# Kernel tuning notes

Measured on AMD Instinct MI355X. Metric: run time of the kernel, lower is better.

## Reference

```python
import jax, jax.numpy as jnp
import numpy as np

B, S, H, I, E, K = 4, 2048, 1024, 4096, 8, 2


def setup_inputs() -> dict:
    key = jax.random.key(0)
    ks = jax.random.split(key, 5)
    scale = 1.0 / np.sqrt(H)
    return {
        "hidden_states": jax.random.normal(ks[0], (B, S, H), dtype=jnp.float32),
        "router_w": jax.random.normal(ks[1], (E, H), dtype=jnp.float32) * scale,
        "gate_w": jax.random.normal(ks[2], (E, I, H), dtype=jnp.float32) * scale,
        "up_w": jax.random.normal(ks[3], (E, I, H), dtype=jnp.float32) * scale,
        "down_w": jax.random.normal(ks[4], (E, H, I), dtype=jnp.float32) * (1.0 / np.sqrt(I)),
        "top_k": K,
    }


def reference(hidden_states, router_w, gate_w, up_w, down_w, top_k):
    # Router: logits -> softmax -> top-k -> renormalized weights (eval mode, no jitter)
    logits = jnp.einsum("bsh,eh->bse", hidden_states, router_w)
    probs = jax.nn.softmax(logits, axis=-1)
    expert_weights, expert_indices = jax.lax.top_k(probs, top_k)  # [B,S,K]
    expert_weights = expert_weights / expert_weights.sum(axis=-1, keepdims=True)

    n_experts = router_w.shape[0]
    # Per-token combine weight for each expert: [B,S,E]
    combine = (jax.nn.one_hot(expert_indices, n_experts, dtype=expert_weights.dtype)
               * expert_weights[..., None]).sum(axis=-2)

    out = jnp.zeros_like(hidden_states)
    for e in range(n_experts):  # fixed small expert count
        g = jax.nn.silu(hidden_states @ gate_w[e].T)  # [B,S,I]
        u = hidden_states @ up_w[e].T                 # [B,S,I]
        y = (g * u) @ down_w[e].T                     # [B,S,H]
        out = out + combine[..., e:e + 1] * y
    return out
```

## Files before the change

### kernel.cpp

```cpp
#include <hip/hip_runtime.h>
#include <hip/hip_bf16.h>
#include <math.h>
#include <stdint.h>

#define TOKENS 8192
#define HD 1024
#define ID 4096
#define NE 8
#define RMAX 18432
#define MAXT 72

typedef __attribute__((ext_vector_type(8))) short short8v;
typedef __attribute__((ext_vector_type(4))) float f32x4;

typedef const __attribute__((address_space(1))) unsigned int* gas_u32p;
typedef __attribute__((address_space(3))) unsigned int* las_u32p;

__device__ __forceinline__ void stage16(const void* g, void* l) {
  __builtin_amdgcn_global_load_lds((gas_u32p)g, (las_u32p)l, 16, 0, 0);
}

#define BARRIER asm volatile("s_barrier" ::: "memory")
#define WAITLGKM asm volatile("s_waitcnt lgkmcnt(0)" ::: "memory")
#define VMC0 asm volatile("s_waitcnt vmcnt(0)" ::: "memory")
#define VMC4 asm volatile("s_waitcnt vmcnt(4)" ::: "memory")
#define VMC6 asm volatile("s_waitcnt vmcnt(6)" ::: "memory")

__global__ __launch_bounds__(256) void convert_kernel(const float* __restrict__ src,
                                                      __hip_bfloat16* __restrict__ dst) {
  size_t i = ((size_t)blockIdx.x * 256 + threadIdx.x) * 8;
  float4 a = ((const float4*)(src + i))[0];
  float4 b = ((const float4*)(src + i))[1];
  union { __hip_bfloat16 h[8]; int4 v; } u;
  u.h[0] = __float2bfloat16(a.x); u.h[1] = __float2bfloat16(a.y);
  u.h[2] = __float2bfloat16(a.z); u.h[3] = __float2bfloat16(a.w);
  u.h[4] = __float2bfloat16(b.x); u.h[5] = __float2bfloat16(b.y);
  u.h[6] = __float2bfloat16(b.z); u.h[7] = __float2bfloat16(b.w);
  *(int4*)(dst + i) = u.v;
}

__global__ __launch_bounds__(256) void router_kernel(
    const float* __restrict__ h, const float* __restrict__ rw,
    __hip_bfloat16* __restrict__ hx, int* __restrict__ tidx,
    float* __restrict__ tw, int* __restrict__ cnt) {
  int wid = threadIdx.x >> 6, lane = threadIdx.x & 63;
  int t = blockIdx.x * 4 + wid;
  const float4* h4 = (const float4*)(h + (size_t)t * HD);
  float x[16];
  {
    float4 xa = h4[lane * 4 + 0], xb = h4[lane * 4 + 1], xc = h4[lane * 4 + 2], xd = h4[lane * 4 + 3];
    x[0] = xa.x; x[1] = xa.y; x[2] = xa.z; x[3] = xa.w;
    x[4] = xb.x; x[5] = xb.y; x[6] = xb.z; x[7] = xb.w;
    x[8] = xc.x; x[9] = xc.y; x[10] = xc.z; x[11] = xc.w;
    x[12] = xd.x; x[13] = xd.y; x[14] = xd.z; x[15] = xd.w;
  }
  union { __hip_bfloat16 hb[16]; int4 v[2]; } u;
#pragma unroll
  for (int j = 0; j < 16; j++) u.hb[j] = __float2bfloat16(x[j]);
  {
    int4* hxp = (int4*)(hx + (size_t)t * HD + lane * 16);
    hxp[0] = u.v[0]; hxp[1] = u.v[1];
  }
  double acc[NE];
#pragma unroll
  for (int e = 0; e < NE; e++) {
    const float4* w4 = (const float4*)(rw + e * HD);
    float4 wa = w4[lane * 4 + 0], wb = w4[lane * 4 + 1], wc = w4[lane * 4 + 2], wd = w4[lane * 4 + 3];
    double s = 0.0;
    s += (double)x[0] * wa.x + (double)x[1] * wa.y + (double)x[2] * wa.z + (double)x[3] * wa.w;
    s += (double)x[4] * wb.x + (double)x[5] * wb.y + (double)x[6] * wb.z + (double)x[7] * wb.w;
    s += (double)x[8] * wc.x + (double)x[9] * wc.y + (double)x[10] * wc.z + (double)x[11] * wc.w;
    s += (double)x[12] * wd.x + (double)x[13] * wd.y + (double)x[14] * wd.z + (double)x[15] * wd.w;
    acc[e] = s;
  }
#pragma unroll
  for (int off = 32; off >= 1; off >>= 1)
#pragma unroll
    for (int e = 0; e < NE; e++) acc[e] += __shfl_xor(acc[e], off, 64);
  if (lane == 0) {
    int i0 = 0; double l0 = acc[0];
#pragma unroll
    for (int e = 1; e < NE; e++) if (acc[e] > l0) { l0 = acc[e]; i0 = e; }
    int i1 = -1; double l1 = -1.0e300;
#pragma unroll
    for (int e = 0; e < NE; e++) if (e != i0 && acc[e] > l1) { l1 = acc[e]; i1 = e; }
    double r = exp(l1 - l0);
    float w0 = (float)(1.0 / (1.0 + r));
    float w1 = (float)(r / (1.0 + r));
    tidx[t * 2 + 0] = i0; tidx[t * 2 + 1] = i1;
    tw[t * 2 + 0] = w0;  tw[t * 2 + 1] = w1;
    atomicAdd(&cnt[i0], 1); atomicAdd(&cnt[i1], 1);
  }
}

__global__ void scan_kernel(const int* __restrict__ cnt, int* __restrict__ ofs, int* __restrict__ cnt2) {
  if (threadIdx.x == 0) {
    int a = 0;
    for (int e = 0; e < NE; e++) { ofs[e] = a; a += (cnt[e] + 255) & ~255; }
    ofs[NE] = a;
  }
  if (threadIdx.x < NE) cnt2[threadIdx.x] = 0;
}

__global__ __launch_bounds__(256) void scatter_kernel(
    const int* __restrict__ tidx, const float* __restrict__ tw,
    const int* __restrict__ ofs, int* __restrict__ cnt2,
    int* __restrict__ rowmap, int* __restrict__ slots) {
  int t = blockIdx.x * 256 + threadIdx.x;
#pragma unroll
  for (int k = 0; k < 2; k++) {
    int e = tidx[t * 2 + k];
    int pos = atomicAdd(&cnt2[e], 1);
    int row = ofs[e] + pos;
    rowmap[row] = t;
    slots[t * 2 + k] = row;
  }
}

__global__ __launch_bounds__(256) void gather_kernel(
    const __hip_bfloat16* __restrict__ hx, const int* __restrict__ rowmap,
    const int* __restrict__ ofs, __hip_bfloat16* __restrict__ A1) {
  int r = blockIdx.x * 4 + (threadIdx.x >> 6);
  int lane = threadIdx.x & 63;
  if (r >= ofs[NE]) return;
  int t = rowmap[r];
  int4* dst = (int4*)(A1 + (size_t)r * HD);
  if (t < 0) {
    int4 z = {0, 0, 0, 0};
    dst[lane * 2 + 0] = z; dst[lane * 2 + 1] = z;
  } else {
    const int4* src = (const int4*)(hx + (size_t)t * HD);
    dst[lane * 2 + 0] = src[lane * 2 + 0];
    dst[lane * 2 + 1] = src[lane * 2 + 1];
  }
}

#define MFMAQ(ACC, MO, NO, AF, BF)                                                         \
  { _Pragma("unroll") for (int m_ = 0; m_ < 4; m_++)                                       \
    _Pragma("unroll") for (int n_ = 0; n_ < 2; n_++)                                       \
    _Pragma("unroll") for (int k_ = 0; k_ < 2; k_++)                                       \
      ACC[(MO) + m_][(NO) + n_] = __builtin_amdgcn_mfma_f32_16x16x32_bf16(                 \
          AF[m_][k_], BF[n_][k_], ACC[(MO) + m_][(NO) + n_], 0, 0, 0); }

__global__ __launch_bounds__(512, 2) void gemm1_kernel(
    const __hip_bfloat16* __restrict__ A1, const __hip_bfloat16* __restrict__ Wg,
    const __hip_bfloat16* __restrict__ Wu, const int* __restrict__ ofs,
    __hip_bfloat16* __restrict__ act) {
  __shared__ __align__(128) char lds[131072];
  const int nwg = gridDim.x;
  int wg0 = blockIdx.x;
  int wg = (wg0 & 7) * (nwg >> 3) + (wg0 >> 3);
  const int tm = wg >> 5, tn = wg & 31;
  const int Rtot = ofs[NE];
  const int row0 = tm * 256;
  if (row0 >= Rtot) return;
  int e = 0;
#pragma unroll
  for (int i = 1; i < NE; i++) e += (row0 >= ofs[i]);
  const int tid = threadIdx.x, wid = tid >> 6, lane = tid & 63;
  const int wm = wid >> 1, wn = wid & 1;
  const int fr = lane & 15, fkE = (lane >> 4) << 3;
  const int wmB = wm * 64, wnB = wn * 64;

  const char* srcA[4]; const char* srcG[2]; const char* srcU[2];
  int ldA[4], ldG[2], ldU[2];
#pragma unroll
  for (int j = 0; j < 4; j++) {
    int d = j * 8192 + tid * 16;
    int row = d >> 7;
    int kb = (d ^ (((d >> 7) & 7) << 4)) & 127;
    srcA[j] = (const char*)(A1 + (size_t)(row0 + row) * HD) + kb;
    ldA[j] = j * 8192 + wid * 1024;
  }
#pragma unroll
  for (int j = 0; j < 2; j++) {
    int d = j * 8192 + tid * 16;
    int row = d >> 7;
    int kb = (d ^ (((d >> 7) & 7) << 4)) & 127;
    srcG[j] = (const char*)(Wg + ((size_t)e * ID + tn * 128 + row) * HD) + kb;
    srcU[j] = (const char*)(Wu + ((size_t)e * ID + tn * 128 + row) * HD) + kb;
    ldG[j] = 32768 + j * 8192 + wid * 1024;
    ldU[j] = 49152 + j * 8192 + wid * 1024;
  }
#define STG_A(j, t, bf) stage16(srcA[j] + (size_t)(t) * 128, (char*)lds + (bf) * 65536 + ldA[j])
#define STG_G(j, t, bf) stage16(srcG[j] + (size_t)(t) * 128, (char*)lds + (bf) * 65536 + ldG[j])
#define STG_U(j, t, bf) stage16(srcU[j] + (size_t)(t) * 128, (char*)lds + (bf) * 65536 + ldU[j])

  auto RD = [&](int bf, int poff, int rowi, int kki) -> short8v {
    int o = ((rowi + fr) << 7) + ((kki << 5) + fkE) * 2;
    o ^= ((o >> 7) & 7) << 4;
    return *(const short8v*)(&lds[bf * 65536 + poff + o]);
  };

  f32x4 accG[4][4], accU[4][4];
#pragma unroll
  for (int m = 0; m < 4; m++)
#pragma unroll
    for (int n = 0; n < 4; n++) { accG[m][n] = (f32x4)(0.0f); accU[m][n] = (f32x4)(0.0f); }

  const int NT = HD / 64;
#pragma unroll
  for (int j = 0; j < 4; j++) STG_A(j, 0, 0);
#pragma unroll
  for (int j = 0; j < 2; j++) STG_G(j, 0, 0);
#pragma unroll
  for (int j = 0; j < 2; j++) STG_U(j, 0, 0);
#pragma unroll
  for (int j = 0; j < 4; j++) STG_A(j, 1, 1);
#pragma unroll
  for (int j = 0; j < 2; j++) STG_G(j, 1, 1);
  VMC6; BARRIER;

#pragma unroll 1
  for (int I = 0; I < NT / 2; ++I) {
    const int t0 = 2 * I;
    const bool more = (t0 + 2 < NT);
    short8v a[4][2], bA[2][2], bB[2][2];
#pragma unroll
    for (int m = 0; m < 4; m++) { a[m][0] = RD(0, 0, wmB + m * 16, 0); a[m][1] = RD(0, 0, wmB + m * 16, 1); }
#pragma unroll
    for (int n = 0; n < 2; n++) { bA[n][0] = RD(0, 32768, wnB + n * 16, 0); bA[n][1] = RD(0, 32768, wnB + n * 16, 1); }
    STG_U(0, t0 + 1, 1); STG_U(1, t0 + 1, 1);
    BARRIER; WAITLGKM;
    __builtin_amdgcn_s_setprio(1); MFMAQ(accG, 0, 0, a, bA); __builtin_amdgcn_s_setprio(0);
    BARRIER;
#pragma unroll
    for (int n = 0; n < 2; n++) { bB[n][0] = RD(0, 32768, wnB + 32 + n * 16, 0); bB[n][1] = RD(0, 32768, wnB + 32 + n * 16, 1); }
    if (more) { STG_A(0, t0 + 2, 0); STG_A(1, t0 + 2, 0); }
    BARRIER; WAITLGKM;
    __builtin_amdgcn_s_setprio(1); MFMAQ(accG, 0, 2, a, bB); __builtin_amdgcn_s_setprio(0);
    BARRIER;
#pragma unroll
    for (int n = 0; n < 2; n++) { bA[n][0] = RD(0, 49152, wnB + n * 16, 0); bA[n][1] = RD(0, 49152, wnB + n * 16, 1); }
    if (more) { STG_A(2, t0 + 2, 0); STG_A(3, t0 + 2, 0); }
    BARRIER; WAITLGKM;
    __builtin_amdgcn_s_setprio(1); MFMAQ(accU, 0, 0, a, bA); __builtin_amdgcn_s_setprio(0);
    BARRIER;
#pragma unroll
    for (int n = 0; n < 2; n++) { bB[n][0] = RD(0, 49152, wnB + 32 + n * 16, 0); bB[n][1] = RD(0, 49152, wnB + 32 + n * 16, 1); }
    if (more) { STG_G(0, t0 + 2, 0); STG_G(1, t0 + 2, 0); }
    BARRIER; WAITLGKM;
    __builtin_amdgcn_s_setprio(1); MFMAQ(accU, 0, 2, a, bB); __builtin_amdgcn_s_setprio(0);
    if (more) { VMC6; } else { VMC0; }
    BARRIER;
#pragma unroll
    for (int m = 0; m < 4; m++) { a[m][0] = RD(1, 0, wmB + m * 16, 0); a[m][1] = RD(1, 0, wmB + m * 16, 1); }
#pragma unroll
    for (int n = 0; n < 2; n++) { bA[n][0] = RD(1, 32768, wnB + n * 16, 0); bA[n][1] = RD(1, 32768, wnB + n * 16, 1); }
    if (more) { STG_U(0, t0 + 2, 0); STG_U(1, t0 + 2, 0); }
    BARRIER; WAITLGKM;
    __builtin_amdgcn_s_setprio(1); MFMAQ(accG, 0, 0, a, bA); __builtin_amdgcn_s_setprio(0);
    BARRIER;
#pragma unroll
    for (int n = 0; n < 2; n++) { bB[n][0] = RD(1, 32768, wnB + 32 + n * 16, 0); bB[n][1] = RD(1, 32768, wnB + 32 + n * 16, 1); }
    if (more) { STG_A(0, t0 + 3, 1); STG_A(1, t0 + 3, 1); }
    BARRIER; WAITLGKM;
    __builtin_amdgcn_s_setprio(1); MFMAQ(accG, 0, 2, a, bB); __builtin_amdgcn_s_setprio(0);
    BARRIER;
#pragma unroll
    for (int n = 0; n < 2; n++) { bA[n][0] = RD(1, 49152, wnB + n * 16, 0); bA[n][1] = RD(1, 49152, wnB + n * 16, 1); }
    if (more) { STG_A(2, t0 + 3, 1); STG_A(3, t0 + 3, 1); }
    BARRIER; WAITLGKM;
    __builtin_amdgcn_s_setprio(1); MFMAQ(accU, 0, 0, a, bA); __builtin_amdgcn_s_setprio(0);
    BARRIER;
#pragma unroll
    for (int n = 0; n < 2; n++) { bB[n][0] = RD(1, 49152, wnB + 32 + n * 16, 0); bB[n][1] = RD(1, 49152, wnB + 32 + n * 16, 1); }
    if (more) { STG_G(0, t0 + 3, 1); STG_G(1, t0 + 3, 1); }
    BARRIER; WAITLGKM;
    __builtin_amdgcn_s_setprio(1); MFMAQ(accU, 0, 2, a, bB); __builtin_amdgcn_s_setprio(0);
    if (more) { VMC6; } else { VMC0; }
    BARRIER;
  }
#undef STG_A
#undef STG_G
#undef STG_U

  const int rb = row0 + wmB + ((lane >> 4) << 2);
  const int cb = tn * 128 + wnB + fr;
#pragma unroll
  for (int m = 0; m < 4; m++)
#pragma unroll
    for (int i = 0; i < 4; i++) {
      int r = rb + m * 16 + i;
      __hip_bfloat16* dst = act + (size_t)r * ID + cb;
#pragma unroll
      for (int n = 0; n < 4; n++) {
        float g = accG[m][n][i], uu = accU[m][n][i];
        float s = g / (1.0f + __expf(-g));
        dst[n * 16] = __float2bfloat16(s * uu);
      }
    }
}

__global__ __launch_bounds__(512, 2) void gemm2_kernel(
    const __hip_bfloat16* __restrict__ act, const __hip_bfloat16* __restrict__ Wd,
    const int* __restrict__ ofs, float* __restrict__ ybuf) {
  __shared__ __align__(128) char lds[131072];
  const int nwg = gridDim.x;
  int wg0 = blockIdx.x;
  int wg = (wg0 & 7) * (nwg >> 3) + (wg0 >> 3);
  const int tm = wg >> 2, tn = wg & 3;
  const int Rtot = ofs[NE];
  const int row0 = tm * 256;
  if (row0 >= Rtot) return;
  int e = 0;
#pragma unroll
  for (int i = 1; i < NE; i++) e += (row0 >= ofs[i]);
  const int tid = threadIdx.x, wid = tid >> 6, lane = tid & 63;
  const int wm = wid >> 2, wn = wid & 3;
  const int fr = lane & 15, fkE = (lane >> 4) << 3;
  const int wmB = wm * 128, wnB = wn * 64;

  const char* srcA[4]; const char* srcB[4];
  int ldA[4], ldB[4];
#pragma unroll
  for (int j = 0; j < 4; j++) {
    int d = j * 8192 + tid * 16;
    int row = d >> 7;
    int kb = (d ^ (((d >> 7) & 7) << 4)) & 127;
    srcA[j] = (const char*)(act + (size_t)(row0 + row) * ID) + kb;
    srcB[j] = (const char*)(Wd + ((size_t)e * HD + tn * 256 + row) * ID) + kb;
    ldA[j] = j * 8192 + wid * 1024;
    ldB[j] = 32768 + j * 8192 + wid * 1024;
  }
#define STG_A2(j, t, bf) stage16(srcA[j] + (size_t)(t) * 128, (char*)lds + (bf) * 65536 + ldA[j])
#define STG_B2(j, t, bf) stage16(srcB[j] + (size_t)(t) * 128, (char*)lds + (bf) * 65536 + ldB[j])

  auto RD = [&](int bf, int poff, int rowi, int kki) -> short8v {
    int o = ((rowi + fr) << 7) + ((kki << 5) + fkE) * 2;
    o ^= ((o >> 7) & 7) << 4;
    return *(const short8v*)(&lds[bf * 65536 + poff + o]);
  };

  f32x4 acc[8][4];
#pragma unroll
  for (int m = 0; m < 8; m++)
#pragma unroll
    for (int n = 0; n < 4; n++) acc[m][n] = (f32x4)(0.0f);

  const int NT = ID / 64;
#pragma unroll
  for (int j = 0; j < 4; j++) STG_B2(j, 0, 0);
#pragma unroll
  for (int j = 0; j < 4; j++) STG_A2(j, 0, 0);
#pragma unroll
  for (int j = 0; j < 4; j++) STG_B2(j, 1, 1);
  VMC4; BARRIER;

#pragma unroll 1
  for (int I = 0; I < NT / 2; ++I) {
    const int t0 = 2 * I;
    const bool more = (t0 + 2 < NT);
    short8v a0[4][2], a1[4][2], b0[2][2], b1[2][2];
#pragma unroll
    for (int m = 0; m < 4; m++) { a0[m][0] = RD(0, 0, wmB + m * 16, 0); a0[m][1] = RD(0, 0, wmB + m * 16, 1); }
#pragma unroll
    for (int n = 0; n < 2; n++) { b0[n][0] = RD(0, 32768, wnB + n * 16, 0); b0[n][1] = RD(0, 32768, wnB + n * 16, 1); }
    STG_A2(0, t0 + 1, 1); STG_A2(1, t0 + 1, 1);
    BARRIER; WAITLGKM;
    __builtin_amdgcn_s_setprio(1); MFMAQ(acc, 0, 0, a0, b0); __builtin_amdgcn_s_setprio(0);
    BARRIER;
#pragma unroll
    for (int n = 0; n < 2; n++) { b1[n][0] = RD(0, 32768, wnB + 32 + n * 16, 0); b1[n][1] = RD(0, 32768, wnB + 32 + n * 16, 1); }
    STG_A2(2, t0 + 1, 1); STG_A2(3, t0 + 1, 1);
    BARRIER; WAITLGKM;
    __builtin_amdgcn_s_setprio(1); MFMAQ(acc, 0, 2, a0, b1); __builtin_amdgcn_s_setprio(0);
    BARRIER;
#pragma unroll
    for (int m = 0; m < 4; m++) { a1[m][0] = RD(0, 0, wmB + 64 + m * 16, 0); a1[m][1] = RD(0, 0, wmB + 64 + m * 16, 1); }
    if (more) { STG_B2(0, t0 + 2, 0); STG_B2(1, t0 + 2, 0); }
    BARRIER; WAITLGKM;
    __builtin_amdgcn_s_setprio(1); MFMAQ(acc, 4, 2, a1, b1); __builtin_amdgcn_s_setprio(0);
    BARRIER;
    if (more) { STG_B2(2, t0 + 2, 0); STG_B2(3, t0 + 2, 0); }
    BARRIER; WAITLGKM;
    __builtin_amdgcn_s_setprio(1); MFMAQ(acc, 4, 0, a1, b0); __builtin_amdgcn_s_setprio(0);
    if (more) { VMC4; } else { VMC0; }
    BARRIER;
#pragma unroll
    for (int m = 0; m < 4; m++) { a0[m][0] = RD(1, 0, wmB + m * 16, 0); a0[m][1] = RD(1, 0, wmB + m * 16, 1); }
#pragma unroll
    for (int n = 0; n < 2; n++) { b0[n][0] = RD(1, 32768, wnB + n * 16, 0); b0[n][1] = RD(1, 32768, wnB + n * 16, 1); }
    if (more) { STG_A2(0, t0 + 2, 0); STG_A2(1, t0 + 2, 0); }
    BARRIER; WAITLGKM;
    __builtin_amdgcn_s_setprio(1); MFMAQ(acc, 0, 0, a0, b0); __builtin_amdgcn_s_setprio(0);
    BARRIER;
#pragma unroll
    for (int n = 0; n < 2; n++) { b1[n][0] = RD(1, 32768, wnB + 32 + n * 16, 0); b1[n][1] = RD(1, 32768, wnB + 32 + n * 16, 1); }
    if (more) { STG_A2(2, t0 + 2, 0); STG_A2(3, t0 + 2, 0); }
    BARRIER; WAITLGKM;
    __builtin_amdgcn_s_setprio(1); MFMAQ(acc, 0, 2, a0, b1); __builtin_amdgcn_s_setprio(0);
    BARRIER;
#pragma unroll
    for (int m = 0; m < 4; m++) { a1[m][0] = RD(1, 0, wmB + 64 + m * 16, 0); a1[m][1] = RD(1, 0, wmB + 64 + m * 16, 1); }
    if (more) { STG_B2(0, t0 + 3, 1); STG_B2(1, t0 + 3, 1); }
    BARRIER; WAITLGKM;
    __builtin_amdgcn_s_setprio(1); MFMAQ(acc, 4, 2, a1, b1); __builtin_amdgcn_s_setprio(0);
    BARRIER;
    if (more) { STG_B2(2, t0 + 3, 1); STG_B2(3, t0 + 3, 1); }
    BARRIER; WAITLGKM;
    __builtin_amdgcn_s_setprio(1); MFMAQ(acc, 4, 0, a1, b0); __builtin_amdgcn_s_setprio(0);
    if (more) { VMC4; } else { VMC0; }
    BARRIER;
  }
#undef STG_A2
#undef STG_B2

  const int rb = row0 + wmB + ((lane >> 4) << 2);
  const int cb = tn * 256 + wnB + fr;
#pragma unroll
  for (int m = 0; m < 8; m++)
#pragma unroll
    for (int i = 0; i < 4; i++) {
      int r = rb + m * 16 + i;
      float* dst = ybuf + (size_t)r * HD + cb;
#pragma unroll
      for (int n = 0; n < 4; n++) dst[n * 16] = acc[m][n][i];
    }
}

__global__ __launch_bounds__(256) void combine_kernel(
    const float* __restrict__ ybuf, const int* __restrict__ slots,
    const float* __restrict__ tw, float* __restrict__ out) {
  int t = blockIdx.x * 4 + (threadIdx.x >> 6);
  int lane = threadIdx.x & 63;
  int r0 = slots[t * 2 + 0], r1 = slots[t * 2 + 1];
  float w0 = tw[t * 2 + 0], w1 = tw[t * 2 + 1];
  const float4* y0 = (const float4*)(ybuf + (size_t)r0 * HD);
  const float4* y1 = (const float4*)(ybuf + (size_t)r1 * HD);
  float4* o = (float4*)(out + (size_t)t * HD);
#pragma unroll
  for (int j = 0; j < 4; j++) {
    int ix = j * 64 + lane;
    float4 a = y0[ix], b = y1[ix];
    float4 c;
    c.x = w0 * a.x + w1 * b.x; c.y = w0 * a.y + w1 * b.y;
    c.z = w0 * a.z + w1 * b.z; c.w = w0 * a.w + w1 * b.w;
    o[ix] = c;
  }
}

extern "C" void kernel_launch(void* const* d_in, const int* in_sizes, int n_in,
                              void* d_out, int out_size, void* d_ws, size_t ws_size,
                              hipStream_t stream) {
  (void)in_sizes; (void)n_in; (void)out_size; (void)ws_size;
  const float* h  = (const float*)d_in[0];
  const float* rw = (const float*)d_in[1];
  const float* gw = (const float*)d_in[2];
  const float* uw = (const float*)d_in[3];
  const float* dw = (const float*)d_in[4];
  float* out = (float*)d_out;

  char* ws = (char*)d_ws;
  size_t off = 0;
  auto alloc = [&](size_t bytes) { char* p = ws + off; off += (bytes + 255) & ~255ULL; return p; };
  __hip_bfloat16* wg  = (__hip_bfloat16*)alloc((size_t)NE * ID * HD * 2);
  __hip_bfloat16* wu  = (__hip_bfloat16*)alloc((size_t)NE * ID * HD * 2);
  __hip_bfloat16* wd  = (__hip_bfloat16*)alloc((size_t)NE * HD * ID * 2);
  __hip_bfloat16* act = (__hip_bfloat16*)alloc((size_t)RMAX * ID * 2);
  size_t hx_off = off;
  __hip_bfloat16* hx  = (__hip_bfloat16*)alloc((size_t)TOKENS * HD * 2);
  __hip_bfloat16* A1  = (__hip_bfloat16*)alloc((size_t)RMAX * HD * 2);
  float* ybuf = (float*)(ws + hx_off);
  {
    size_t yend = hx_off + (size_t)RMAX * HD * 4;
    if (yend > off) off = (yend + 255) & ~255ULL;
  }
  int* rowmap = (int*)alloc(RMAX * 4);
  int* tidx   = (int*)alloc(TOKENS * 2 * 4);
  float* twt  = (float*)alloc(TOKENS * 2 * 4);
  int* slots  = (int*)alloc(TOKENS * 2 * 4);
  int* cnt    = (int*)alloc(256);
  int* cnt2   = (int*)alloc(256);
  int* ofs    = (int*)alloc(256);

  hipMemsetAsync(cnt, 0, NE * 4, stream);
  hipMemsetAsync(rowmap, 0xFF, RMAX * 4, stream);

  convert_kernel<<<16384, 256, 0, stream>>>(gw, wg);
  convert_kernel<<<16384, 256, 0, stream>>>(uw, wu);
  convert_kernel<<<16384, 256, 0, stream>>>(dw, wd);
  router_kernel<<<TOKENS / 4, 256, 0, stream>>>(h, rw, hx, tidx, twt, cnt);
  scan_kernel<<<1, 64, 0, stream>>>(cnt, ofs, cnt2);
  scatter_kernel<<<TOKENS / 256, 256, 0, stream>>>(tidx, twt, ofs, cnt2, rowmap, slots);
  gather_kernel<<<RMAX / 4, 256, 0, stream>>>(hx, rowmap, ofs, A1);
  gemm1_kernel<<<MAXT * 32, 512, 0, stream>>>(A1, wg, wu, ofs, act);
  gemm2_kernel<<<MAXT * 4, 512, 0, stream>>>(act, wd, ofs, ybuf);
  combine_kernel<<<TOKENS / 4, 256, 0, stream>>>(ybuf, slots, twt, out);
}
```

Baseline: 925.4 us.

## Fuse row gather into gemm1 A loads and shrink gemm2 N tile

Removes the gather kernel and the A1 buffer: gemm1 now builds its A-tile source pointers directly from rowmap into hx, with padded rows pointing at a zeroed row. gemm2's output tile drops from 256x256 to 256x128 with 8 waves in a 4x2 layout. That doubles the grid, halves the accumulators and cuts LDS to 96KB, and its staging pipeline is restructured around a vmcnt(3) wait. The aim is to save one kernel launch plus a full copy of the gathered activations, and to improve gemm2 occupancy and load balance. The cost is that gemm2 rereads the activation tiles from global memory twice as often.

```diff
diff --git a/kernel.cpp b/kernel.cpp
--- a/kernel.cpp
+++ b/kernel.cpp
@@ -23,7 +23,7 @@
 #define BARRIER asm volatile("s_barrier" ::: "memory")
 #define WAITLGKM asm volatile("s_waitcnt lgkmcnt(0)" ::: "memory")
 #define VMC0 asm volatile("s_waitcnt vmcnt(0)" ::: "memory")
-#define VMC4 asm volatile("s_waitcnt vmcnt(4)" ::: "memory")
+#define VMC3 asm volatile("s_waitcnt vmcnt(3)" ::: "memory")
 #define VMC6 asm volatile("s_waitcnt vmcnt(6)" ::: "memory")
 
 __global__ __launch_bounds__(256) void convert_kernel(const float* __restrict__ src,
@@ -117,24 +117,6 @@
   }
 }
 
-__global__ __launch_bounds__(256) void gather_kernel(
-    const __hip_bfloat16* __restrict__ hx, const int* __restrict__ rowmap,
-    const int* __restrict__ ofs, __hip_bfloat16* __restrict__ A1) {
-  int r = blockIdx.x * 4 + (threadIdx.x >> 6);
-  int lane = threadIdx.x & 63;
-  if (r >= ofs[NE]) return;
-  int t = rowmap[r];
-  int4* dst = (int4*)(A1 + (size_t)r * HD);
-  if (t < 0) {
-    int4 z = {0, 0, 0, 0};
-    dst[lane * 2 + 0] = z; dst[lane * 2 + 1] = z;
-  } else {
-    const int4* src = (const int4*)(hx + (size_t)t * HD);
-    dst[lane * 2 + 0] = src[lane * 2 + 0];
-    dst[lane * 2 + 1] = src[lane * 2 + 1];
-  }
-}
-
 #define MFMAQ(ACC, MO, NO, AF, BF)                                                         \
   { _Pragma("unroll") for (int m_ = 0; m_ < 4; m_++)                                       \
     _Pragma("unroll") for (int n_ = 0; n_ < 2; n_++)                                       \
@@ -143,8 +125,9 @@
           AF[m_][k_], BF[n_][k_], ACC[(MO) + m_][(NO) + n_], 0, 0, 0); }
 
 __global__ __launch_bounds__(512, 2) void gemm1_kernel(
-    const __hip_bfloat16* __restrict__ A1, const __hip_bfloat16* __restrict__ Wg,
-    const __hip_bfloat16* __restrict__ Wu, const int* __restrict__ ofs,
+    const __hip_bfloat16* __restrict__ hx, const __hip_bfloat16* __restrict__ Wg,
+    const __hip_bfloat16* __restrict__ Wu, const int* __restrict__ rowmap,
+    const int* __restrict__ ofs, const __hip_bfloat16* __restrict__ zrow,
     __hip_bfloat16* __restrict__ act) {
   __shared__ __align__(128) char lds[131072];
   const int nwg = gridDim.x;
@@ -169,7 +152,9 @@
     int d = j * 8192 + tid * 16;
     int row = d >> 7;
     int kb = (d ^ (((d >> 7) & 7) << 4)) & 127;
-    srcA[j] = (const char*)(A1 + (size_t)(row0 + row) * HD) + kb;
+    int tok = rowmap[row0 + row];
+    const __hip_bfloat16* base = (tok >= 0) ? (hx + (size_t)tok * HD) : zrow;
+    srcA[j] = (const char*)base + kb;
     ldA[j] = j * 8192 + wid * 1024;
   }
 #pragma unroll
@@ -295,11 +280,11 @@
 __global__ __launch_bounds__(512, 2) void gemm2_kernel(
     const __hip_bfloat16* __restrict__ act, const __hip_bfloat16* __restrict__ Wd,
     const int* __restrict__ ofs, float* __restrict__ ybuf) {
-  __shared__ __align__(128) char lds[131072];
+  __shared__ __align__(128) char lds[98304];
   const int nwg = gridDim.x;
   int wg0 = blockIdx.x;
   int wg = (wg0 & 7) * (nwg >> 3) + (wg0 >> 3);
-  const int tm = wg >> 2, tn = wg & 3;
+  const int tm = wg >> 3, tn = wg & 7;
   const int Rtot = ofs[NE];
   const int row0 = tm * 256;
   if (row0 >= Rtot) return;
@@ -307,109 +292,93 @@
 #pragma unroll
   for (int i = 1; i < NE; i++) e += (row0 >= ofs[i]);
   const int tid = threadIdx.x, wid = tid >> 6, lane = tid & 63;
-  const int wm = wid >> 2, wn = wid & 3;
+  const int wm = wid >> 1, wn = wid & 1;
   const int fr = lane & 15, fkE = (lane >> 4) << 3;
-  const int wmB = wm * 128, wnB = wn * 64;
-
-  const char* srcA[4]; const char* srcB[4];
-  int ldA[4], ldB[4];
+  const int wmB = wm * 64, wnB = wn * 64;
+
+  const char* srcA[4]; const char* srcB[2];
+  int ldA[4], ldB[2];
 #pragma unroll
   for (int j = 0; j < 4; j++) {
     int d = j * 8192 + tid * 16;
     int row = d >> 7;
     int kb = (d ^ (((d >> 7) & 7) << 4)) & 127;
     srcA[j] = (const char*)(act + (size_t)(row0 + row) * ID) + kb;
-    srcB[j] = (const char*)(Wd + ((size_t)e * HD + tn * 256 + row) * ID) + kb;
     ldA[j] = j * 8192 + wid * 1024;
+  }
+#pragma unroll
+  for (int j = 0; j < 2; j++) {
+    int d = j * 8192 + tid * 16;
+    int row = d >> 7;
+    int kb = (d ^ (((d >> 7) & 7) << 4)) & 127;
+    srcB[j] = (const char*)(Wd + ((size_t)e * HD + tn * 128 + row) * ID) + kb;
     ldB[j] = 32768 + j * 8192 + wid * 1024;
   }
-#define STG_A2(j, t, bf) stage16(srcA[j] + (size_t)(t) * 128, (char*)lds + (bf) * 65536 + ldA[j])
-#define STG_B2(j, t, bf) stage16(srcB[j] + (size_t)(t) * 128, (char*)lds + (bf) * 65536 + ldB[j])
+#define STG_A2(j, t, bf) stage16(srcA[j] + (size_t)(t) * 128, (char*)lds + (bf) * 49152 + ldA[j])
+#define STG_B2(j, t, bf) stage16(srcB[j] + (size_t)(t) * 128, (char*)lds + (bf) * 49152 + ldB[j])
 
   auto RD = [&](int bf, int poff, int rowi, int kki) -> short8v {
     int o = ((rowi + fr) << 7) + ((kki << 5) + fkE) * 2;
     o ^= ((o >> 7) & 7) << 4;
-    return *(const short8v*)(&lds[bf * 65536 + poff + o]);
+    return *(const short8v*)(&lds[bf * 49152 + poff + o]);
   };
 
-  f32x4 acc[8][4];
-#pragma unroll
-  for (int m = 0; m < 8; m++)
+  f32x4 acc[4][4];
+#pragma unroll
+  for (int m = 0; m < 4; m++)
 #pragma unroll
     for (int n = 0; n < 4; n++) acc[m][n] = (f32x4)(0.0f);
 
   const int NT = ID / 64;
 #pragma unroll
-  for (int j = 0; j < 4; j++) STG_B2(j, 0, 0);
-#pragma unroll
   for (int j = 0; j < 4; j++) STG_A2(j, 0, 0);
-#pragma unroll
-  for (int j = 0; j < 4; j++) STG_B2(j, 1, 1);
-  VMC4; BARRIER;
+  STG_B2(0, 0, 0); STG_B2(1, 0, 0);
+  STG_A2(0, 1, 1); STG_A2(1, 1, 1); STG_A2(2, 1, 1);
+  VMC3; BARRIER;
 
 #pragma unroll 1
   for (int I = 0; I < NT / 2; ++I) {
-    const int t0 = 2 * I;
-    const bool more = (t0 + 2 < NT);
-    short8v a0[4][2], a1[4][2], b0[2][2], b1[2][2];
-#pragma unroll
-    for (int m = 0; m < 4; m++) { a0[m][0] = RD(0, 0, wmB + m * 16, 0); a0[m][1] = RD(0, 0, wmB + m * 16, 1); }
+    const int T = 2 * I;
+    const bool more = (T + 2 < NT);
+    short8v a[4][2], b0[2][2], b1[2][2];
+#pragma unroll
+    for (int m = 0; m < 4; m++) { a[m][0] = RD(0, 0, wmB + m * 16, 0); a[m][1] = RD(0, 0, wmB + m * 16, 1); }
 #pragma unroll
     for (int n = 0; n < 2; n++) { b0[n][0] = RD(0, 32768, wnB + n * 16, 0); b0[n][1] = RD(0, 32768, wnB + n * 16, 1); }
-    STG_A2(0, t0 + 1, 1); STG_A2(1, t0 + 1, 1);
-    BARRIER; WAITLGKM;
-    __builtin_amdgcn_s_setprio(1); MFMAQ(acc, 0, 0, a0, b0); __builtin_amdgcn_s_setprio(0);
+    STG_A2(3, T + 1, 1); STG_B2(0, T + 1, 1); STG_B2(1, T + 1, 1);
+    BARRIER; WAITLGKM;
+    __builtin_amdgcn_s_setprio(1); MFMAQ(acc, 0, 0, a, b0); __builtin_amdgcn_s_setprio(0);
     BARRIER;
 #pragma unroll
     for (int n = 0; n < 2; n++) { b1[n][0] = RD(0, 32768, wnB + 32 + n * 16, 0); b1[n][1] = RD(0, 32768, wnB + 32 + n * 16, 1); }
-    STG_A2(2, t0 + 1, 1); STG_A2(3, t0 + 1, 1);
-    BARRIER; WAITLGKM;
-    __builtin_amdgcn_s_setprio(1); MFMAQ(acc, 0, 2, a0, b1); __builtin_amdgcn_s_setprio(0);
-    BARRIER;
-#pragma unroll
-    for (int m = 0; m < 4; m++) { a1[m][0] = RD(0, 0, wmB + 64 + m * 16, 0); a1[m][1] = RD(0, 0, wmB + 64 + m * 16, 1); }
-    if (more) { STG_B2(0, t0 + 2, 0); STG_B2(1, t0 + 2, 0); }
-    BARRIER; WAITLGKM;
-    __builtin_amdgcn_s_setprio(1); MFMAQ(acc, 4, 2, a1, b1); __builtin_amdgcn_s_setprio(0);
-    BARRIER;
-    if (more) { STG_B2(2, t0 + 2, 0); STG_B2(3, t0 + 2, 0); }
-    BARRIER; WAITLGKM;
-    __builtin_amdgcn_s_setprio(1); MFMAQ(acc, 4, 0, a1, b0); __builtin_amdgcn_s_setprio(0);
-    if (more) { VMC4; } else { VMC0; }
-    BARRIER;
-#pragma unroll
-    for (int m = 0; m < 4; m++) { a0[m][0] = RD(1, 0, wmB + m * 16, 0); a0[m][1] = RD(1, 0, wmB + m * 16, 1); }
+    if (more) { STG_A2(0, T + 2, 0); STG_A2(1, T + 2, 0); STG_A2(2, T + 2, 0); }
+    BARRIER; WAITLGKM;
+    __builtin_amdgcn_s_setprio(1); MFMAQ(acc, 0, 2, a, b1); __builtin_amdgcn_s_setprio(0);
+    if (more) { VMC3; } else { VMC0; }
+    BARRIER;
+#pragma unroll
+    for (int m = 0; m < 4; m++) { a[m][0] = RD(1, 0, wmB + m * 16, 0); a[m][1] = RD(1, 0, wmB + m * 16, 1); }
 #pragma unroll
     for (int n = 0; n < 2; n++) { b0[n][0] = RD(1, 32768, wnB + n * 16, 0); b0[n][1] = RD(1, 32768, wnB + n * 16, 1); }
-    if (more) { STG_A2(0, t0 + 2, 0); STG_A2(1, t0 + 2, 0); }
-    BARRIER; WAITLGKM;
-    __builtin_amdgcn_s_setprio(1); MFMAQ(acc, 0, 0, a0, b0); __builtin_amdgcn_s_setprio(0);
+    if (more) { STG_A2(3, T + 2, 0); STG_B2(0, T + 2, 0); STG_B2(1, T + 2, 0); }
+    BARRIER; WAITLGKM;
+    __builtin_amdgcn_s_setprio(1); MFMAQ(acc, 0, 0, a, b0); __builtin_amdgcn_s_setprio(0);
     BARRIER;
 #pragma unroll
     for (int n = 0; n < 2; n++) { b1[n][0] = RD(1, 32768, wnB + 32 + n * 16, 0); b1[n][1] = RD(1, 32768, wnB + 32 + n * 16, 1); }
-    if (more) { STG_A2(2, t0 + 2, 0); STG_A2(3, t0 + 2, 0); }
-    BARRIER; WAITLGKM;
-    __builtin_amdgcn_s_setprio(1); MFMAQ(acc, 0, 2, a0, b1); __builtin_amdgcn_s_setprio(0);
-    BARRIER;
-#pragma unroll
-    for (int m = 0; m < 4; m++) { a1[m][0] = RD(1, 0, wmB + 64 + m * 16, 0); a1[m][1] = RD(1, 0, wmB + 64 + m * 16, 1); }
-    if (more) { STG_B2(0, t0 + 3, 1); STG_B2(1, t0 + 3, 1); }
-    BARRIER; WAITLGKM;
-    __builtin_amdgcn_s_setprio(1); MFMAQ(acc, 4, 2, a1, b1); __builtin_amdgcn_s_setprio(0);
-    BARRIER;
-    if (more) { STG_B2(2, t0 + 3, 1); STG_B2(3, t0 + 3, 1); }
-    BARRIER; WAITLGKM;
-    __builtin_amdgcn_s_setprio(1); MFMAQ(acc, 4, 0, a1, b0); __builtin_amdgcn_s_setprio(0);
-    if (more) { VMC4; } else { VMC0; }
+    if (more) { STG_A2(0, T + 3, 1); STG_A2(1, T + 3, 1); STG_A2(2, T + 3, 1); }
+    BARRIER; WAITLGKM;
+    __builtin_amdgcn_s_setprio(1); MFMAQ(acc, 0, 2, a, b1); __builtin_amdgcn_s_setprio(0);
+    if (more) { VMC3; } else { VMC0; }
     BARRIER;
   }
 #undef STG_A2
 #undef STG_B2
 
   const int rb = row0 + wmB + ((lane >> 4) << 2);
-  const int cb = tn * 256 + wnB + fr;
-#pragma unroll
-  for (int m = 0; m < 8; m++)
+  const int cb = tn * 128 + wnB + fr;
+#pragma unroll
+  for (int m = 0; m < 4; m++)
 #pragma unroll
     for (int i = 0; i < 4; i++) {
       int r = rb + m * 16 + i;
@@ -458,14 +427,9 @@
   __hip_bfloat16* wu  = (__hip_bfloat16*)alloc((size_t)NE * ID * HD * 2);
   __hip_bfloat16* wd  = (__hip_bfloat16*)alloc((size_t)NE * HD * ID * 2);
   __hip_bfloat16* act = (__hip_bfloat16*)alloc((size_t)RMAX * ID * 2);
-  size_t hx_off = off;
   __hip_bfloat16* hx  = (__hip_bfloat16*)alloc((size_t)TOKENS * HD * 2);
-  __hip_bfloat16* A1  = (__hip_bfloat16*)alloc((size_t)RMAX * HD * 2);
-  float* ybuf = (float*)(ws + hx_off);
-  {
-    size_t yend = hx_off + (size_t)RMAX * HD * 4;
-    if (yend > off) off = (yend + 255) & ~255ULL;
-  }
+  float* ybuf = (float*)alloc((size_t)RMAX * HD * 4);
+  __hip_bfloat16* zrow = (__hip_bfloat16*)alloc(HD * 2);
   int* rowmap = (int*)alloc(RMAX * 4);
   int* tidx   = (int*)alloc(TOKENS * 2 * 4);
   float* twt  = (float*)alloc(TOKENS * 2 * 4);
@@ -476,6 +440,7 @@
 
   hipMemsetAsync(cnt, 0, NE * 4, stream);
   hipMemsetAsync(rowmap, 0xFF, RMAX * 4, stream);
+  hipMemsetAsync(zrow, 0, HD * 2, stream);
 
   convert_kernel<<<16384, 256, 0, stream>>>(gw, wg);
   convert_kernel<<<16384, 256, 0, stream>>>(uw, wu);
@@ -483,8 +448,7 @@
   router_kernel<<<TOKENS / 4, 256, 0, stream>>>(h, rw, hx, tidx, twt, cnt);
   scan_kernel<<<1, 64, 0, stream>>>(cnt, ofs, cnt2);
   scatter_kernel<<<TOKENS / 256, 256, 0, stream>>>(tidx, twt, ofs, cnt2, rowmap, slots);
-  gather_kernel<<<RMAX / 4, 256, 0, stream>>>(hx, rowmap, ofs, A1);
-  gemm1_kernel<<<MAXT * 32, 512, 0, stream>>>(A1, wg, wu, ofs, act);
-  gemm2_kernel<<<MAXT * 4, 512, 0, stream>>>(act, wd, ofs, ybuf);
+  gemm1_kernel<<<MAXT * 32, 512, 0, stream>>>(hx, wg, wu, rowmap, ofs, zrow, act);
+  gemm2_kernel<<<MAXT * 8, 512, 0, stream>>>(act, wd, ofs, ybuf);
   combine_kernel<<<TOKENS / 4, 256, 0, stream>>>(ybuf, slots, twt, out);
 }
```

Measured after the change: 898.1 us. 2.9% less time.
